# Kernel tuning notes

Measured on AMD Instinct MI355X. Metric: run time of the kernel, lower is better.

Reference implementation:

```python
import jax, jax.numpy as jnp
import numpy as np

T, B = 1024, 32
Q1, K1, V1 = 1024, 1024, 1024
Q2, K2, V2 = 1024, 1024, 1024
KW = 3  # kernel_width
EPS = 1e-6


def mask_softmax(x, mask):
    # softmax over dim 0 with multiplicative mask (exp(x-max)*mask / sum)
    e = jnp.exp(x - jnp.max(x, axis=0, keepdims=True))
    e = e * mask
    return e / jnp.sum(e, axis=0, keepdims=True)


def setup_inputs() -> dict:
    key = jax.random.key(0)
    ks = jax.random.split(key, 16)
    s = 0.02
    return {
        "q1": jax.random.normal(ks[0], (B, Q1), jnp.float32),
        "k1": jax.random.normal(ks[1], (T, B, K1), jnp.float32),
        "v1": jax.random.normal(ks[2], (T, B, V1), jnp.float32),
        "q2": jax.random.normal(ks[3], (B, Q2), jnp.float32),
        "k2": jax.random.normal(ks[4], (T, B, K2), jnp.float32),
        "v2": jax.random.normal(ks[5], (T, B, V2), jnp.float32),
        "k_mask": jnp.ones((T, B), jnp.float32),
        # Attention params: sa: Linear(q1_size -> align_size=K1); a1: Linear(K1 -> 1)
        "sa_w": jax.random.normal(ks[6], (K1, Q1), jnp.float32) * s,
        "sa_b": jnp.zeros((K1,), jnp.float32),
        "a1_w": jax.random.normal(ks[7], (1, K1), jnp.float32) * s,
        "a1_b": jnp.zeros((1,), jnp.float32),
        # AttCNN4Weight: q_to_kernel: Linear(q2_size -> k2_size*KW)
        "qk_w": jax.random.normal(ks[8], (K2 * KW, Q2), jnp.float32) * s,
        "qk_b": jnp.zeros((K2 * KW,), jnp.float32),
        # LayerNorm(v1_size)
        "ln_g": jnp.ones((V1,), jnp.float32),
        "ln_b": jnp.zeros((V1,), jnp.float32),
    }


def reference(q1, k1, v1, q2, k2, v2, k_mask,
              sa_w, sa_b, a1_w, a1_b, qk_w, qk_b, ln_g, ln_b):
    # ---- additive attention path ----
    # tanh(sa(q1)[None] + k1): [T, B, K1]
    t = jnp.tanh((q1 @ sa_w.T + sa_b)[None, :, :] + k1)
    a_1 = jnp.einsum('tba,a->tb', t, a1_w[0]) + a1_b[0]          # [T, B]
    e_1 = mask_softmax(a_1, k_mask)
    attend_1 = jnp.einsum('tb,tbd->bd', e_1, v1)                  # [B, V1]

    # ---- dynamic grouped-conv1d attention path ----
    kernel = (q2 @ qk_w.T + qk_b).reshape(B, K2, KW)              # per-example kernels
    pad = (KW - 1) // 2
    k2p = jnp.pad(k2, ((pad, pad), (0, 0), (0, 0)))               # [T+2p, B, K2]
    a_2 = jnp.zeros((T, B), k2.dtype)
    for w in range(KW):  # tiny fixed loop over kernel taps
        a_2 = a_2 + jnp.einsum('tbc,bc->tb', k2p[w:w + T], kernel[:, :, w])
    e_2 = mask_softmax(a_2, k_mask)
    attend_2 = jnp.einsum('tb,tbd->bd', e_2, v2)                  # [B, V2]

    # ---- combine: add + LayerNorm over feature dim ----
    x = attend_1 + attend_2
    mu = jnp.mean(x, axis=-1, keepdims=True)
    var = jnp.mean((x - mu) ** 2, axis=-1, keepdims=True)
    combined = (x - mu) * jax.lax.rsqrt(var + EPS) * ln_g + ln_b
    return combined
```

## Files before the change

kernel.cpp:

```cpp
#include <hip/hip_runtime.h>
#include <math.h>

#define T_DIM   1024
#define B_DIM   32
#define N_FEAT  1024
#define KW      3
#define NT      32
#define T_PER   (T_DIM / NT)
#define TT      32
#define EPS     1e-6f

__device__ __forceinline__ float tanh_fast(float x) {
  float ax = fminf(fabsf(x), 10.f);
  float e  = __expf(ax + ax);
  float r  = fmaf(-2.f, __builtin_amdgcn_rcpf(e + 1.f), 1.f);
  return copysignf(r, x);
}

__global__ void __launch_bounds__(256) prep_kernel(
    const float* __restrict__ q1, const float* __restrict__ sa_w,
    const float* __restrict__ sa_b, const float* __restrict__ q2,
    const float* __restrict__ qk_w, const float* __restrict__ qk_b,
    float* __restrict__ sa_q, float* __restrict__ kern_t) {
  int wid  = (blockIdx.x * 256 + threadIdx.x) >> 6;
  int lane = threadIdx.x & 63;
  int b = wid & (B_DIM - 1);
  int m = wid >> 5;
  const float4* xr;
  const float4* wr;
  if (m < 1024) {
    xr = (const float4*)(q1 + (size_t)b * N_FEAT);
    wr = (const float4*)(sa_w + (size_t)m * N_FEAT);
  } else {
    xr = (const float4*)(q2 + (size_t)b * N_FEAT);
    wr = (const float4*)(qk_w + (size_t)(m - 1024) * N_FEAT);
  }
  float acc = 0.f;
#pragma unroll
  for (int i = 0; i < 4; i++) {
    float4 xv = xr[lane + 64 * i], wv = wr[lane + 64 * i];
    acc += xv.x * wv.x + xv.y * wv.y + xv.z * wv.z + xv.w * wv.w;
  }
#pragma unroll
  for (int off = 32; off > 0; off >>= 1) acc += __shfl_down(acc, off, 64);
  if (lane == 0) {
    if (m < 1024) {
      sa_q[(size_t)b * N_FEAT + m] = acc + sa_b[m];
    } else {
      int mm = m - 1024;
      int c = mm / 3, w = mm - 3 * c;
      kern_t[(size_t)b * (N_FEAT * KW) + (size_t)w * N_FEAT + c] = acc + qk_b[mm];
    }
  }
}

__global__ void __launch_bounds__(256, 4) row_dots_kernel(
    const float* __restrict__ k1, const float* __restrict__ k2,
    const float* __restrict__ sa_q, const float* __restrict__ a1_w,
    const float* __restrict__ kern_t, const float* __restrict__ a1_b,
    float* __restrict__ a1_out, float* __restrict__ s_out) {
  int b   = blockIdx.x;
  int t0  = blockIdx.y * TT;
  int tid = threadIdx.x, wave = tid >> 6, lane = tid & 63;

  __shared__ float kw_s[KW][N_FEAT];
  __shared__ float sq_s[N_FEAT];
  __shared__ float aw_s[N_FEAT];
  {
    const float4* src = (const float4*)(kern_t + (size_t)b * (N_FEAT * KW));
    float4* dst = (float4*)&kw_s[0][0];
#pragma unroll
    for (int i = 0; i < 3; i++) dst[tid + 256 * i] = src[tid + 256 * i];
    ((float4*)sq_s)[tid] = ((const float4*)(sa_q + (size_t)b * N_FEAT))[tid];
    ((float4*)aw_s)[tid] = ((const float4*)a1_w)[tid];
  }
  __syncthreads();
  float a1bv = a1_b[0];

  float4 c1[4], c2[4];
  {
    size_t rb = ((size_t)(t0 + wave) * B_DIM + b) * N_FEAT;
#pragma unroll
    for (int ch = 0; ch < 4; ch++) {
      c1[ch] = *(const float4*)(k1 + rb + ch * 256 + lane * 4);
      c2[ch] = *(const float4*)(k2 + rb + ch * 256 + lane * 4);
    }
  }
  for (int i = 0; i < TT / 4; i++) {
    int t = t0 + 4 * i + wave;
    float4 n1[4], n2[4];
    if (i + 1 < TT / 4) {
      size_t nb = ((size_t)(t + 4) * B_DIM + b) * N_FEAT;
#pragma unroll
      for (int ch = 0; ch < 4; ch++) {
        n1[ch] = *(const float4*)(k1 + nb + ch * 256 + lane * 4);
        n2[ch] = *(const float4*)(k2 + nb + ch * 256 + lane * 4);
      }
    } else {
#pragma unroll
      for (int ch = 0; ch < 4; ch++) { n1[ch] = c1[ch]; n2[ch] = c2[ch]; }
    }
    float p1 = 0.f, s0 = 0.f, s1 = 0.f, s2 = 0.f;
#pragma unroll
    for (int ch = 0; ch < 4; ch++) {
      int f = ch * 256 + lane * 4;
      float4 A  = c1[ch], Bv = c2[ch];
      float4 sq = *(const float4*)&sq_s[f];
      float4 aw = *(const float4*)&aw_s[f];
      p1 += tanh_fast(A.x + sq.x) * aw.x;
      p1 += tanh_fast(A.y + sq.y) * aw.y;
      p1 += tanh_fast(A.z + sq.z) * aw.z;
      p1 += tanh_fast(A.w + sq.w) * aw.w;
      float4 w0 = *(const float4*)&kw_s[0][f];
      float4 w1 = *(const float4*)&kw_s[1][f];
      float4 w2 = *(const float4*)&kw_s[2][f];
      s0 += Bv.x * w0.x + Bv.y * w0.y + Bv.z * w0.z + Bv.w * w0.w;
      s1 += Bv.x * w1.x + Bv.y * w1.y + Bv.z * w1.z + Bv.w * w1.w;
      s2 += Bv.x * w2.x + Bv.y * w2.y + Bv.z * w2.z + Bv.w * w2.w;
    }
#pragma unroll
    for (int off = 32; off > 0; off >>= 1) {
      p1 += __shfl_xor(p1, off, 64);
      s0 += __shfl_xor(s0, off, 64);
      s1 += __shfl_xor(s1, off, 64);
      s2 += __shfl_xor(s2, off, 64);
    }
    if (lane == 0) {
      size_t o = (size_t)t * B_DIM + b;
      a1_out[o] = p1 + a1bv;
      s_out[o * 3 + 0] = s0;
      s_out[o * 3 + 1] = s1;
      s_out[o * 3 + 2] = s2;
    }
#pragma unroll
    for (int ch = 0; ch < 4; ch++) { c1[ch] = n1[ch]; c2[ch] = n2[ch]; }
  }
}

__device__ __forceinline__ float block_reduce_256(float v, bool is_max,
                                                  float* sm ) {
#pragma unroll
  for (int off = 32; off > 0; off >>= 1) {
    float o = __shfl_down(v, off, 64);
    v = is_max ? fmaxf(v, o) : v + o;
  }
  int wave = threadIdx.x >> 6;
  if ((threadIdx.x & 63) == 0) sm[wave] = v;
  __syncthreads();
  float r = is_max ? fmaxf(fmaxf(sm[0], sm[1]), fmaxf(sm[2], sm[3]))
                   : sm[0] + sm[1] + sm[2] + sm[3];
  __syncthreads();
  return r;
}

__global__ void __launch_bounds__(256) softmax_kernel(
    const float* __restrict__ a1, const float* __restrict__ s,
    const float* __restrict__ k_mask,
    float* __restrict__ e1, float* __restrict__ e2) {
  int b = blockIdx.x;
  int tid = threadIdx.x;
  __shared__ float sm[4];

  float x1[4], x2[4], mk[4];
#pragma unroll
  for (int k = 0; k < 4; k++) {
    int t = tid + k * 256;
    x1[k] = a1[(size_t)t * B_DIM + b];
    float sl = (t > 0)         ? s[((size_t)(t - 1) * B_DIM + b) * 3 + 0] : 0.f;
    float sc =                   s[((size_t)t       * B_DIM + b) * 3 + 1];
    float sr = (t < T_DIM - 1) ? s[((size_t)(t + 1) * B_DIM + b) * 3 + 2] : 0.f;
    x2[k] = sl + sc + sr;
    mk[k] = k_mask[(size_t)t * B_DIM + b];
  }
  float m1 = fmaxf(fmaxf(x1[0], x1[1]), fmaxf(x1[2], x1[3]));
  float m2 = fmaxf(fmaxf(x2[0], x2[1]), fmaxf(x2[2], x2[3]));
  m1 = block_reduce_256(m1, true, sm);
  m2 = block_reduce_256(m2, true, sm);

  float v1[4], v2[4], sum1 = 0.f, sum2 = 0.f;
#pragma unroll
  for (int k = 0; k < 4; k++) {
    v1[k] = __expf(x1[k] - m1) * mk[k];
    v2[k] = __expf(x2[k] - m2) * mk[k];
    sum1 += v1[k];
    sum2 += v2[k];
  }
  sum1 = block_reduce_256(sum1, false, sm);
  sum2 = block_reduce_256(sum2, false, sm);
  float i1 = 1.f / sum1, i2 = 1.f / sum2;
#pragma unroll
  for (int k = 0; k < 4; k++) {
    int t = tid + k * 256;
    e1[(size_t)t * B_DIM + b] = v1[k] * i1;
    e2[(size_t)t * B_DIM + b] = v2[k] * i2;
  }
}

__global__ void __launch_bounds__(256) weighted_v_kernel(
    const float* __restrict__ v1, const float* __restrict__ v2,
    const float* __restrict__ e1, const float* __restrict__ e2,
    float* __restrict__ partial) {
  int b  = blockIdx.x;
  int tc = blockIdx.y;
  int tid = threadIdx.x;
  __shared__ float se1[T_PER], se2[T_PER];
  if (tid < T_PER)
    se1[tid] = e1[(size_t)(tc * T_PER + tid) * B_DIM + b];
  else if (tid < 2 * T_PER)
    se2[tid - T_PER] = e2[(size_t)(tc * T_PER + (tid - T_PER)) * B_DIM + b];
  __syncthreads();

  float4 acc1 = {0.f, 0.f, 0.f, 0.f}, acc2 = {0.f, 0.f, 0.f, 0.f};
  size_t dofs = (size_t)tid * 4;
#pragma unroll 8
  for (int i = 0; i < T_PER; i++) {
    size_t row = ((size_t)(tc * T_PER + i) * B_DIM + b) * N_FEAT + dofs;
    float4 a = *(const float4*)(v1 + row);
    float4 c = *(const float4*)(v2 + row);
    float w1 = se1[i], w2 = se2[i];
    acc1.x = fmaf(w1, a.x, acc1.x); acc1.y = fmaf(w1, a.y, acc1.y);
    acc1.z = fmaf(w1, a.z, acc1.z); acc1.w = fmaf(w1, a.w, acc1.w);
    acc2.x = fmaf(w2, c.x, acc2.x); acc2.y = fmaf(w2, c.y, acc2.y);
    acc2.z = fmaf(w2, c.z, acc2.z); acc2.w = fmaf(w2, c.w, acc2.w);
  }
  size_t o1 = ((size_t)(0 * NT + tc) * B_DIM + b) * N_FEAT + dofs;
  size_t o2 = ((size_t)(1 * NT + tc) * B_DIM + b) * N_FEAT + dofs;
  *(float4*)(partial + o1) = acc1;
  *(float4*)(partial + o2) = acc2;
}

__device__ __forceinline__ float block_reduce_sum_1024(float v, float* sm) {
#pragma unroll
  for (int off = 32; off > 0; off >>= 1) v += __shfl_down(v, off, 64);
  int wave = threadIdx.x >> 6;
  if ((threadIdx.x & 63) == 0) sm[wave] = v;
  __syncthreads();
  float tot = 0.f;
#pragma unroll
  for (int i = 0; i < 16; i++) tot += sm[i];
  __syncthreads();
  return tot;
}

__global__ void __launch_bounds__(1024) ln_kernel(
    const float* __restrict__ partial, const float* __restrict__ ln_g,
    const float* __restrict__ ln_b, float* __restrict__ out) {
  int b = blockIdx.x;
  int d = threadIdx.x;
  __shared__ float sm[16];
  float x = 0.f;
#pragma unroll
  for (int j = 0; j < 2 * NT; j++)
    x += partial[((size_t)j * B_DIM + b) * N_FEAT + d];
  float ssum = block_reduce_sum_1024(x, sm);
  float mu = ssum * (1.f / N_FEAT);
  float dx = x - mu;
  float vsum = block_reduce_sum_1024(dx * dx, sm);
  float inv = rsqrtf(vsum * (1.f / N_FEAT) + EPS);
  out[(size_t)b * N_FEAT + d] = dx * inv * ln_g[d] + ln_b[d];
}

extern "C" void kernel_launch(void* const* d_in, const int* in_sizes, int n_in,
                              void* d_out, int out_size, void* d_ws, size_t ws_size,
                              hipStream_t stream) {
  const float* q1     = (const float*)d_in[0];
  const float* k1     = (const float*)d_in[1];
  const float* v1     = (const float*)d_in[2];
  const float* q2     = (const float*)d_in[3];
  const float* k2     = (const float*)d_in[4];
  const float* v2     = (const float*)d_in[5];
  const float* k_mask = (const float*)d_in[6];
  const float* sa_w   = (const float*)d_in[7];
  const float* sa_b   = (const float*)d_in[8];
  const float* a1_w   = (const float*)d_in[9];
  const float* a1_b   = (const float*)d_in[10];
  const float* qk_w   = (const float*)d_in[11];
  const float* qk_b   = (const float*)d_in[12];
  const float* ln_g   = (const float*)d_in[13];
  const float* ln_bp  = (const float*)d_in[14];
  float* out = (float*)d_out;
  float* ws  = (float*)d_ws;
  (void)k_mask;

  float* sa_q    = ws;
  float* kern_t  = sa_q + 32768;
  float* s       = kern_t + 98304;
  float* a1      = s + 98304;
  float* e1      = a1 + 32768;
  float* e2      = e1 + 32768;
  float* partial = e2 + 32768;

  prep_kernel<<<dim3((4096 * B_DIM) / 4), 256, 0, stream>>>(
      q1, sa_w, sa_b, q2, qk_w, qk_b, sa_q, kern_t);
  row_dots_kernel<<<dim3(B_DIM, T_DIM / TT), 256, 0, stream>>>(
      k1, k2, sa_q, a1_w, kern_t, a1_b, a1, s);
  softmax_kernel<<<dim3(B_DIM), 256, 0, stream>>>(a1, s, k_mask, e1, e2);
  weighted_v_kernel<<<dim3(B_DIM, NT), 256, 0, stream>>>(v1, v2, e1, e2, partial);
  ln_kernel<<<dim3(B_DIM), 1024, 0, stream>>>(partial, ln_g, ln_bp, out);
}
```

Measured before the change: 554.8 us.

## Use one block per (t,b) row in row_dots instead of LDS-staged tiles

Rewrites row_dots_kernel so each 256-thread block handles a single (t,b) row. The launch grows from 1024 to 32768 blocks. The per-batch kernel weights, sa_q and a1_w are no longer staged in shared memory; every block reads them straight from global memory/cache. The explicit register double-buffered prefetch of the next rows is removed. The goal is more parallelism and memory-level concurrency for streaming k1/k2, at the cost of many more redundant weight loads, a block-wide reduction per row, and much larger launch and scheduling overhead.

```diff
diff --git a/kernel.cpp b/kernel.cpp
--- a/kernel.cpp
+++ b/kernel.cpp
@@ -7,7 +7,6 @@
 #define KW      3
 #define NT      32
 #define T_PER   (T_DIM / NT)
-#define TT      32
 #define EPS     1e-6f
 
 __device__ __forceinline__ float tanh_fast(float x) {
@@ -54,86 +53,56 @@
   }
 }
 
-__global__ void __launch_bounds__(256, 4) row_dots_kernel(
+__global__ void __launch_bounds__(256) row_dots_kernel(
     const float* __restrict__ k1, const float* __restrict__ k2,
     const float* __restrict__ sa_q, const float* __restrict__ a1_w,
     const float* __restrict__ kern_t, const float* __restrict__ a1_b,
     float* __restrict__ a1_out, float* __restrict__ s_out) {
-  int b   = blockIdx.x;
-  int t0  = blockIdx.y * TT;
-  int tid = threadIdx.x, wave = tid >> 6, lane = tid & 63;
-
-  __shared__ float kw_s[KW][N_FEAT];
-  __shared__ float sq_s[N_FEAT];
-  __shared__ float aw_s[N_FEAT];
-  {
-    const float4* src = (const float4*)(kern_t + (size_t)b * (N_FEAT * KW));
-    float4* dst = (float4*)&kw_s[0][0];
-#pragma unroll
-    for (int i = 0; i < 3; i++) dst[tid + 256 * i] = src[tid + 256 * i];
-    ((float4*)sq_s)[tid] = ((const float4*)(sa_q + (size_t)b * N_FEAT))[tid];
-    ((float4*)aw_s)[tid] = ((const float4*)a1_w)[tid];
-  }
-  __syncthreads();
-  float a1bv = a1_b[0];
-
-  float4 c1[4], c2[4];
-  {
-    size_t rb = ((size_t)(t0 + wave) * B_DIM + b) * N_FEAT;
-#pragma unroll
-    for (int ch = 0; ch < 4; ch++) {
-      c1[ch] = *(const float4*)(k1 + rb + ch * 256 + lane * 4);
-      c2[ch] = *(const float4*)(k2 + rb + ch * 256 + lane * 4);
-    }
-  }
-  for (int i = 0; i < TT / 4; i++) {
-    int t = t0 + 4 * i + wave;
-    float4 n1[4], n2[4];
-    if (i + 1 < TT / 4) {
-      size_t nb = ((size_t)(t + 4) * B_DIM + b) * N_FEAT;
-#pragma unroll
-      for (int ch = 0; ch < 4; ch++) {
-        n1[ch] = *(const float4*)(k1 + nb + ch * 256 + lane * 4);
-        n2[ch] = *(const float4*)(k2 + nb + ch * 256 + lane * 4);
-      }
-    } else {
-#pragma unroll
-      for (int ch = 0; ch < 4; ch++) { n1[ch] = c1[ch]; n2[ch] = c2[ch]; }
-    }
-    float p1 = 0.f, s0 = 0.f, s1 = 0.f, s2 = 0.f;
-#pragma unroll
-    for (int ch = 0; ch < 4; ch++) {
-      int f = ch * 256 + lane * 4;
-      float4 A  = c1[ch], Bv = c2[ch];
-      float4 sq = *(const float4*)&sq_s[f];
-      float4 aw = *(const float4*)&aw_s[f];
-      p1 += tanh_fast(A.x + sq.x) * aw.x;
-      p1 += tanh_fast(A.y + sq.y) * aw.y;
-      p1 += tanh_fast(A.z + sq.z) * aw.z;
-      p1 += tanh_fast(A.w + sq.w) * aw.w;
-      float4 w0 = *(const float4*)&kw_s[0][f];
-      float4 w1 = *(const float4*)&kw_s[1][f];
-      float4 w2 = *(const float4*)&kw_s[2][f];
-      s0 += Bv.x * w0.x + Bv.y * w0.y + Bv.z * w0.z + Bv.w * w0.w;
-      s1 += Bv.x * w1.x + Bv.y * w1.y + Bv.z * w1.z + Bv.w * w1.w;
-      s2 += Bv.x * w2.x + Bv.y * w2.y + Bv.z * w2.z + Bv.w * w2.w;
-    }
-#pragma unroll
-    for (int off = 32; off > 0; off >>= 1) {
-      p1 += __shfl_xor(p1, off, 64);
-      s0 += __shfl_xor(s0, off, 64);
-      s1 += __shfl_xor(s1, off, 64);
-      s2 += __shfl_xor(s2, off, 64);
-    }
-    if (lane == 0) {
-      size_t o = (size_t)t * B_DIM + b;
-      a1_out[o] = p1 + a1bv;
-      s_out[o * 3 + 0] = s0;
-      s_out[o * 3 + 1] = s1;
-      s_out[o * 3 + 2] = s2;
-    }
-#pragma unroll
-    for (int ch = 0; ch < 4; ch++) { c1[ch] = n1[ch]; c2[ch] = n2[ch]; }
+  int blk = blockIdx.x;
+  int b   = blk & (B_DIM - 1);
+  int tid = threadIdx.x;
+  size_t row = (size_t)blk * N_FEAT + tid * 4;
+  int f = tid * 4;
+
+  float4 k1v = *(const float4*)(k1 + row);
+  float4 sqv = *(const float4*)(sa_q + (size_t)b * N_FEAT + f);
+  float4 awv = *(const float4*)(a1_w + f);
+  float p1 = tanh_fast(k1v.x + sqv.x) * awv.x
+           + tanh_fast(k1v.y + sqv.y) * awv.y
+           + tanh_fast(k1v.z + sqv.z) * awv.z
+           + tanh_fast(k1v.w + sqv.w) * awv.w;
+
+  float4 k2v = *(const float4*)(k2 + row);
+  const float* kb = kern_t + (size_t)b * (N_FEAT * KW);
+  float4 w0 = *(const float4*)(kb + 0 * N_FEAT + f);
+  float4 w1 = *(const float4*)(kb + 1 * N_FEAT + f);
+  float4 w2 = *(const float4*)(kb + 2 * N_FEAT + f);
+  float s0 = k2v.x * w0.x + k2v.y * w0.y + k2v.z * w0.z + k2v.w * w0.w;
+  float s1 = k2v.x * w1.x + k2v.y * w1.y + k2v.z * w1.z + k2v.w * w1.w;
+  float s2 = k2v.x * w2.x + k2v.y * w2.y + k2v.z * w2.z + k2v.w * w2.w;
+
+  float vals[4] = {p1, s0, s1, s2};
+#pragma unroll
+  for (int off = 32; off > 0; off >>= 1) {
+#pragma unroll
+    for (int j = 0; j < 4; j++) vals[j] += __shfl_down(vals[j], off, 64);
+  }
+  __shared__ float red[4][4];
+  int wave = tid >> 6, lane = tid & 63;
+  if (lane == 0) {
+#pragma unroll
+    for (int j = 0; j < 4; j++) red[wave][j] = vals[j];
+  }
+  __syncthreads();
+  if (tid == 0) {
+    float r0 = red[0][0] + red[1][0] + red[2][0] + red[3][0];
+    float r1 = red[0][1] + red[1][1] + red[2][1] + red[3][1];
+    float r2 = red[0][2] + red[1][2] + red[2][2] + red[3][2];
+    float r3 = red[0][3] + red[1][3] + red[2][3] + red[3][3];
+    a1_out[blk] = r0 + a1_b[0];
+    s_out[(size_t)blk * 3 + 0] = r1;
+    s_out[(size_t)blk * 3 + 1] = r2;
+    s_out[(size_t)blk * 3 + 2] = r3;
   }
 }
 
@@ -280,7 +249,6 @@
   const float* ln_bp  = (const float*)d_in[14];
   float* out = (float*)d_out;
   float* ws  = (float*)d_ws;
-  (void)k_mask;
 
   float* sa_q    = ws;
   float* kern_t  = sa_q + 32768;
@@ -292,7 +260,7 @@
 
   prep_kernel<<<dim3((4096 * B_DIM) / 4), 256, 0, stream>>>(
       q1, sa_w, sa_b, q2, qk_w, qk_b, sa_q, kern_t);
-  row_dots_kernel<<<dim3(B_DIM, T_DIM / TT), 256, 0, stream>>>(
+  row_dots_kernel<<<dim3(T_DIM * B_DIM), 256, 0, stream>>>(
       k1, k2, sa_q, a1_w, kern_t, a1_b, a1, s);
   softmax_kernel<<<dim3(B_DIM), 256, 0, stream>>>(a1, s, k_mask, e1, e2);
   weighted_v_kernel<<<dim3(B_DIM, NT), 256, 0, stream>>>(v1, v2, e1, e2, partial);
```

Result: faster. 538.1 us (-3.0%).
